# Kernel tuning notes

Measured on AMD Instinct MI355X. Metric: run time of the kernel, lower is better.

Reference implementation:

```python
import jax, jax.numpy as jnp
import numpy as np

MARGIN = 1.0
EPS = 1e-12


def setup_inputs() -> dict:
    key = jax.random.key(0)
    k1, k2 = jax.random.split(key)
    embeddings = jax.random.normal(k1, (4096, 768), dtype=jnp.float32)
    labels = jax.random.randint(k2, (4096,), 0, 4, dtype=jnp.int64)
    return {"embeddings": embeddings, "labels": labels}


def reference(embeddings, labels):
    # F.normalize(p=2, dim=1): x / max(||x||, eps)
    norm = jnp.linalg.norm(embeddings, axis=1, keepdims=True)
    e = embeddings / jnp.maximum(norm, EPS)

    # Euclidean pairwise distance matrix (not squared)
    dot = e @ e.T                                  # [N, N]
    sq = jnp.diagonal(dot)                         # [N]
    dist = sq[None, :] - 2.0 * dot + sq[:, None]
    dist = jnp.sqrt(jnp.maximum(dist, 0.0) + EPS)  # [N, N]

    # Masks: positives = same label, off-diagonal; negatives = different label
    n = labels.shape[0]
    eq = labels[None, :] == labels[:, None]
    pos_mask = eq & ~jnp.eye(n, dtype=bool)
    neg_mask = ~eq

    # Batch-hard mining: per-anchor hardest positive (masked max) and
    # hardest negative (masked min) -- replaces the per-row Python loop.
    d_ap = jnp.max(jnp.where(pos_mask, dist, -jnp.inf), axis=1)  # [N]
    d_an = jnp.min(jnp.where(neg_mask, dist, jnp.inf), axis=1)   # [N]

    valid = jnp.any(pos_mask, axis=1)  # anchors with at least one positive
    per_anchor = jnp.maximum(d_ap - d_an + MARGIN, 0.0)
    per_anchor = jnp.where(valid, per_anchor, 0.0)
    n_valid = jnp.maximum(jnp.sum(valid.astype(jnp.float32)), 1.0)
    return jnp.sum(per_anchor) / n_valid
```

## Files before the change

### kernel.cpp

```cpp
#include <hip/hip_runtime.h>
#include <math.h>

#define N 4096
#define D 768
#define MARGIN 1.0f
#define NTILE 1056
#define NKT 24
#define NSLOT 64

typedef _Float16 half8 __attribute__((ext_vector_type(8)));
typedef _Float16 half4 __attribute__((ext_vector_type(4)));
typedef float f32x4 __attribute__((ext_vector_type(4)));

__device__ __forceinline__ void gl2lds16(const void* g, void* l) {
    __builtin_amdgcn_global_load_lds((const __attribute__((address_space(1))) void*)g,
                                     (__attribute__((address_space(3))) void*)l, 16, 0, 0);
}

template<int Nv>
__device__ __forceinline__ void wait_vm() {
    if constexpr (Nv == 0)      asm volatile("s_waitcnt vmcnt(0)" ::: "memory");
    else if constexpr (Nv == 3) asm volatile("s_waitcnt vmcnt(3)" ::: "memory");
    else                        asm volatile("s_waitcnt vmcnt(6)" ::: "memory");
}

__global__ __launch_bounds__(256) void normalize_kernel(const float* __restrict__ x,
                                                        _Float16* __restrict__ e,
                                                        float* __restrict__ sq,
                                                        float* __restrict__ ap_part,
                                                        float* __restrict__ an_part,
                                                        float* __restrict__ acc,
                                                        unsigned* __restrict__ counter) {
    const int tid = threadIdx.x;
    const int wave = tid >> 6, lane = tid & 63;
    const int row = blockIdx.x * 4 + wave;

    const float4* xr = (const float4*)(x + (size_t)row * D);
    float4 f0 = xr[lane];
    float4 f1 = xr[lane + 64];
    float4 f2 = xr[lane + 128];

    float s = f0.x*f0.x + f0.y*f0.y + f0.z*f0.z + f0.w*f0.w
            + f1.x*f1.x + f1.y*f1.y + f1.z*f1.z + f1.w*f1.w
            + f2.x*f2.x + f2.y*f2.y + f2.z*f2.z + f2.w*f2.w;
    #pragma unroll
    for (int off = 1; off < 64; off <<= 1) s += __shfl_xor(s, off, 64);

    float scale = 1.0f / fmaxf(sqrtf(s), 1e-12f);

    half4* er = (half4*)(e + (size_t)row * D);
    half4 h0 = { (_Float16)(f0.x*scale), (_Float16)(f0.y*scale), (_Float16)(f0.z*scale), (_Float16)(f0.w*scale) };
    half4 h1 = { (_Float16)(f1.x*scale), (_Float16)(f1.y*scale), (_Float16)(f1.z*scale), (_Float16)(f1.w*scale) };
    half4 h2 = { (_Float16)(f2.x*scale), (_Float16)(f2.y*scale), (_Float16)(f2.z*scale), (_Float16)(f2.w*scale) };
    er[lane]       = h0;
    er[lane + 64]  = h1;
    er[lane + 128] = h2;

    if (lane == 0) sq[row] = s * scale * scale;

    int g = blockIdx.x * 256 + tid;
    ap_part[g] = 0.0f;
    an_part[g] = INFINITY;

    if (blockIdx.x == 0 && tid == 0) { acc[0] = 0.f; acc[1] = 0.f; *counter = 0u; }
}

__device__ __forceinline__ void stage_tile(const _Float16* __restrict__ e,
                                           int i0, int j0, int k0,
                                           unsigned short* Sb, int tid, int w) {
    #pragma unroll
    for (int p = 0; p < 2; ++p) {
        int s  = p * 256 + tid;
        int r  = s >> 2;
        int kg = (s & 3) ^ ((r >> 1) & 3);
        gl2lds16(e + (size_t)(i0 + r) * D + k0 + kg * 8,
                 (char*)Sb + (p * 256 + w * 64) * 16);
    }
    {
        int s  = tid;
        int r  = s >> 2;
        int kg = (s & 3) ^ ((r >> 1) & 3);
        gl2lds16(e + (size_t)(j0 + r) * D + k0 + kg * 8,
                 (char*)Sb + 8192 + (w * 64) * 16);
    }
}

__global__ __launch_bounds__(256, 4) void mine_kernel(const _Float16* __restrict__ e,
                                                      const float* __restrict__ sq,
                                                      const int* __restrict__ labels,
                                                      float* __restrict__ ap_part,
                                                      float* __restrict__ an_part) {
    __shared__ unsigned short S[3 * 6144];

    const int tid  = threadIdx.x;
    const int w    = tid >> 6;
    const int lane = tid & 63;
    const int ln15 = lane & 15;
    const int lq   = lane >> 4;
    const int wr   = w >> 1, wc = w & 1;
    const int wi   = wr * 64, wjL = wc * 32;

    const int b = (blockIdx.x & 7) * 132 + (blockIdx.x >> 3);

    int bi = 0, rem = b;
    while (rem >= 64 - 2 * bi) { rem -= 64 - 2 * bi; ++bi; }
    const int cj = 2 * bi + rem;
    const bool diag = (rem <= 1);
    const int i0 = bi * 128, j0 = cj * 64;

    f32x4 acc[4][2] = {};

    stage_tile(e, i0, j0, 0,  S,        tid, w);
    stage_tile(e, i0, j0, 32, S + 6144, tid, w);

    int cur = 0, nx2 = 2;
    for (int kt = 0; kt < NKT; ++kt) {
        if (kt < NKT - 1) wait_vm<3>(); else wait_vm<0>();
        __builtin_amdgcn_s_barrier();
        __builtin_amdgcn_sched_barrier(0);

        if (kt + 2 < NKT)
            stage_tile(e, i0, j0, (kt + 2) * 32, S + nx2 * 6144, tid, w);
        __builtin_amdgcn_sched_barrier(0);

        const unsigned short* Sb = S + cur * 6144;
        half8 af[4], bf[2];
        #pragma unroll
        for (int mt = 0; mt < 4; ++mt) {
            int r  = wi + mt * 16 + ln15;
            int kx = lq ^ ((r >> 1) & 3);
            af[mt] = *(const half8*)&Sb[r * 32 + kx * 8];
        }
        #pragma unroll
        for (int nt = 0; nt < 2; ++nt) {
            int c  = wjL + nt * 16 + ln15;
            int kx = lq ^ ((c >> 1) & 3);
            bf[nt] = *(const half8*)&Sb[4096 + c * 32 + kx * 8];
        }
        __builtin_amdgcn_s_setprio(1);
        #pragma unroll
        for (int mt = 0; mt < 4; ++mt)
            #pragma unroll
            for (int nt = 0; nt < 2; ++nt)
                acc[mt][nt] = __builtin_amdgcn_mfma_f32_16x16x32_f16(af[mt], bf[nt], acc[mt][nt], 0, 0, 0);
        __builtin_amdgcn_s_setprio(0);

        cur = (cur == 2) ? 0 : cur + 1;
        nx2 = (nx2 == 2) ? 0 : nx2 + 1;
    }

    float sqi[4][4]; int labi[4][4];
    #pragma unroll
    for (int mt = 0; mt < 4; ++mt)
        #pragma unroll
        for (int rg = 0; rg < 4; ++rg) {
            int i = i0 + wi + mt * 16 + lq * 4 + rg;
            sqi[mt][rg] = sq[i];
            labi[mt][rg] = labels[i];
        }
    float sqj[2]; int labj[2];
    #pragma unroll
    for (int nt = 0; nt < 2; ++nt) {
        int j = j0 + wjL + nt * 16 + ln15;
        sqj[nt] = sq[j];
        labj[nt] = labels[j];
    }

    float api[4][4], ani[4][4], apj[2], anj[2];
    #pragma unroll
    for (int mt = 0; mt < 4; ++mt)
        #pragma unroll
        for (int rg = 0; rg < 4; ++rg) { api[mt][rg] = -INFINITY; ani[mt][rg] = INFINITY; }
    #pragma unroll
    for (int nt = 0; nt < 2; ++nt) { apj[nt] = -INFINITY; anj[nt] = INFINITY; }

    #pragma unroll
    for (int nt = 0; nt < 2; ++nt) {
        int j = j0 + wjL + nt * 16 + ln15;
        #pragma unroll
        for (int mt = 0; mt < 4; ++mt)
            #pragma unroll
            for (int rg = 0; rg < 4; ++rg) {
                int i = i0 + wi + mt * 16 + lq * 4 + rg;
                float d2 = sqi[mt][rg] + sqj[nt] - 2.0f * acc[mt][nt][rg];
                float dist = sqrtf(fmaxf(d2, 0.0f) + 1e-12f);
                if (labi[mt][rg] == labj[nt]) {
                    if (i != j) {
                        api[mt][rg] = fmaxf(api[mt][rg], dist);
                        apj[nt]     = fmaxf(apj[nt], dist);
                    }
                } else {
                    ani[mt][rg] = fminf(ani[mt][rg], dist);
                    anj[nt]     = fminf(anj[nt], dist);
                }
            }
    }

    float* F = (float*)S;

    #pragma unroll
    for (int mt = 0; mt < 4; ++mt)
        #pragma unroll
        for (int rg = 0; rg < 4; ++rg) {
            float a_ = api[mt][rg], n_ = ani[mt][rg];
            #pragma unroll
            for (int off = 1; off < 16; off <<= 1) {
                a_ = fmaxf(a_, __shfl_xor(a_, off, 64));
                n_ = fminf(n_, __shfl_xor(n_, off, 64));
            }
            if (ln15 == 0) {
                int rl = mt * 16 + lq * 4 + rg;
                F[w * 128 + rl * 2]     = a_;
                F[w * 128 + rl * 2 + 1] = n_;
            }
        }
    __syncthreads();
    if (tid < 128) {
        int half = tid >> 6, rl = tid & 63;
        float a_ = fmaxf(F[(2 * half) * 128 + rl * 2],     F[(2 * half + 1) * 128 + rl * 2]);
        float n_ = fminf(F[(2 * half) * 128 + rl * 2 + 1], F[(2 * half + 1) * 128 + rl * 2 + 1]);
        int row = i0 + half * 64 + rl;
        ap_part[(size_t)cj * N + row] = a_;
        an_part[(size_t)cj * N + row] = n_;
    }

    if (!diag) {
        __syncthreads();
        #pragma unroll
        for (int nt = 0; nt < 2; ++nt) {
            float a_ = apj[nt], n_ = anj[nt];
            #pragma unroll
            for (int off = 16; off < 64; off <<= 1) {
                a_ = fmaxf(a_, __shfl_xor(a_, off, 64));
                n_ = fminf(n_, __shfl_xor(n_, off, 64));
            }
            if (lq == 0) {
                int jl = nt * 16 + ln15;
                F[w * 128 + jl * 2]     = a_;
                F[w * 128 + jl * 2 + 1] = n_;
            }
        }
        __syncthreads();
        if (tid < 64) {
            int wc2 = tid >> 5, jl = tid & 31;
            float a_ = fmaxf(F[wc2 * 128 + jl * 2],     F[(wc2 + 2) * 128 + jl * 2]);
            float n_ = fminf(F[wc2 * 128 + jl * 2 + 1], F[(wc2 + 2) * 128 + jl * 2 + 1]);
            int col = j0 + wc2 * 32 + jl;
            ap_part[(size_t)bi * N + col] = a_;
            an_part[(size_t)bi * N + col] = n_;
        }
    }
}

__global__ __launch_bounds__(256) void reduce_kernel(const float* __restrict__ ap_part,
                                                     const float* __restrict__ an_part,
                                                     const int* __restrict__ labels,
                                                     float* __restrict__ acc,
                                                     unsigned* __restrict__ counter,
                                                     float* __restrict__ out) {
    const int tid = threadIdx.x;
    const int rl  = tid & 63;
    const int q   = tid >> 6;
    const int r   = blockIdx.x * 64 + rl;

    __shared__ int cnt[4];
    __shared__ float Fa[4][64], Fn[4][64];
    if (tid < 4) cnt[tid] = 0;
    __syncthreads();
    int local[4] = {0, 0, 0, 0};
    for (int i = tid; i < N; i += 256) local[labels[i] & 3]++;
    #pragma unroll
    for (int c = 0; c < 4; c++) if (local[c]) atomicAdd(&cnt[c], local[c]);

    float ap = 0.0f, an = INFINITY;
    #pragma unroll
    for (int s = 0; s < 16; ++s) {
        int slot = q * 16 + s;
        ap = fmaxf(ap, ap_part[(size_t)slot * N + r]);
        an = fminf(an, an_part[(size_t)slot * N + r]);
    }
    Fa[q][rl] = ap; Fn[q][rl] = an;
    __syncthreads();

    if (tid < 64) {
        float a_ = fmaxf(fmaxf(Fa[0][tid], Fa[1][tid]), fmaxf(Fa[2][tid], Fa[3][tid]));
        float n_ = fminf(fminf(Fn[0][tid], Fn[1][tid]), fminf(Fn[2][tid], Fn[3][tid]));
        int row = blockIdx.x * 64 + tid;
        int l = labels[row] & 3;
        float sum = 0.f, nv = 0.f;
        if (cnt[l] >= 2) {
            nv = 1.f;
            if (n_ < 3.0e38f) sum = fmaxf(a_ - n_ + MARGIN, 0.f);
        }
        #pragma unroll
        for (int off = 32; off; off >>= 1) {
            sum += __shfl_down(sum, off, 64);
            nv  += __shfl_down(nv,  off, 64);
        }
        if (tid == 0) {
            atomicAdd(&acc[0], sum);
            atomicAdd(&acc[1], nv);
            __threadfence();
            if (atomicAdd(counter, 1u) == 63u) {
                float s_ = atomicAdd(&acc[0], 0.f);
                float nn = atomicAdd(&acc[1], 0.f);
                out[0] = s_ / fmaxf(nn, 1.f);
            }
        }
    }
}

extern "C" void kernel_launch(void* const* d_in, const int* in_sizes, int n_in,
                              void* d_out, int out_size, void* d_ws, size_t ws_size,
                              hipStream_t stream) {
    const float* x = (const float*)d_in[0];
    const int* labels = (const int*)d_in[1];
    float* out = (float*)d_out;

    _Float16* e = (_Float16*)d_ws;
    float* sq = (float*)(e + (size_t)N * D);
    float* ap_part = sq + N;
    float* an_part = ap_part + (size_t)NSLOT * N;
    float* acc = an_part + (size_t)NSLOT * N;
    unsigned* counter = (unsigned*)(acc + 2);

    normalize_kernel<<<N / 4, 256, 0, stream>>>(x, e, sq, ap_part, an_part, acc, counter);
    mine_kernel<<<NTILE, 256, 0, stream>>>(e, sq, labels, ap_part, an_part);
    reduce_kernel<<<N / 64, 256, 0, stream>>>(ap_part, an_part, labels, acc, counter, out);
}
```

Baseline: 116.5 us.

## Enlarge mining tiles to 128x128 with 8 waves and a 4-stage load pipeline

The mining kernel now covers the upper triangle with square 128x128 tiles computed by 512-thread blocks, instead of 128x64 tiles with 256 threads. This halves the tile count and the number of partial slots, and increases operand reuse per staged K-slice. The LDS ring grows from 3 to 4 buffers with a deeper prefetch distance, and the wait counts are adjusted to match. Because every partial slot is now written by either a row or a column write-back, the normalize kernel no longer initialises the partial buffers. In exchange, LDS use per block rises to 64KB and register pressure rises, which may limit how many blocks fit on each CU.

```diff
diff --git a/kernel.cpp b/kernel.cpp
--- a/kernel.cpp
+++ b/kernel.cpp
@@ -4,9 +4,9 @@
 #define N 4096
 #define D 768
 #define MARGIN 1.0f
-#define NTILE 1056
+#define NTILE 528
 #define NKT 24
-#define NSLOT 64
+#define NSLOT 32
 
 typedef _Float16 half8 __attribute__((ext_vector_type(8)));
 typedef _Float16 half4 __attribute__((ext_vector_type(4)));
@@ -20,15 +20,13 @@
 template<int Nv>
 __device__ __forceinline__ void wait_vm() {
     if constexpr (Nv == 0)      asm volatile("s_waitcnt vmcnt(0)" ::: "memory");
-    else if constexpr (Nv == 3) asm volatile("s_waitcnt vmcnt(3)" ::: "memory");
-    else                        asm volatile("s_waitcnt vmcnt(6)" ::: "memory");
+    else if constexpr (Nv == 2) asm volatile("s_waitcnt vmcnt(2)" ::: "memory");
+    else                        asm volatile("s_waitcnt vmcnt(4)" ::: "memory");
 }
 
 __global__ __launch_bounds__(256) void normalize_kernel(const float* __restrict__ x,
                                                         _Float16* __restrict__ e,
                                                         float* __restrict__ sq,
-                                                        float* __restrict__ ap_part,
-                                                        float* __restrict__ an_part,
                                                         float* __restrict__ acc,
                                                         unsigned* __restrict__ counter) {
     const int tid = threadIdx.x;
@@ -57,73 +55,68 @@
     er[lane + 128] = h2;
 
     if (lane == 0) sq[row] = s * scale * scale;
-
-    int g = blockIdx.x * 256 + tid;
-    ap_part[g] = 0.0f;
-    an_part[g] = INFINITY;
-
     if (blockIdx.x == 0 && tid == 0) { acc[0] = 0.f; acc[1] = 0.f; *counter = 0u; }
 }
 
 __device__ __forceinline__ void stage_tile(const _Float16* __restrict__ e,
                                            int i0, int j0, int k0,
-                                           unsigned short* Sb, int tid, int w) {
-    #pragma unroll
-    for (int p = 0; p < 2; ++p) {
-        int s  = p * 256 + tid;
-        int r  = s >> 2;
-        int kg = (s & 3) ^ ((r >> 1) & 3);
+                                           unsigned short* Sb, int tid) {
+    {
+        int r  = tid >> 2;
+        int kg = (tid & 3) ^ ((r >> 1) & 3);
         gl2lds16(e + (size_t)(i0 + r) * D + k0 + kg * 8,
-                 (char*)Sb + (p * 256 + w * 64) * 16);
+                 (char*)Sb + tid * 16);
     }
     {
-        int s  = tid;
-        int r  = s >> 2;
-        int kg = (s & 3) ^ ((r >> 1) & 3);
+        int r  = tid >> 2;
+        int kg = (tid & 3) ^ ((r >> 1) & 3);
         gl2lds16(e + (size_t)(j0 + r) * D + k0 + kg * 8,
-                 (char*)Sb + 8192 + (w * 64) * 16);
-    }
-}
-
-__global__ __launch_bounds__(256, 4) void mine_kernel(const _Float16* __restrict__ e,
+                 (char*)Sb + 8192 + tid * 16);
+    }
+}
+
+__global__ __launch_bounds__(512, 4) void mine_kernel(const _Float16* __restrict__ e,
                                                       const float* __restrict__ sq,
                                                       const int* __restrict__ labels,
                                                       float* __restrict__ ap_part,
                                                       float* __restrict__ an_part) {
-    __shared__ unsigned short S[3 * 6144];
+    __shared__ unsigned short S[4 * 8192];
 
     const int tid  = threadIdx.x;
     const int w    = tid >> 6;
     const int lane = tid & 63;
     const int ln15 = lane & 15;
     const int lq   = lane >> 4;
-    const int wr   = w >> 1, wc = w & 1;
+    const int wr   = w >> 2, wc = w & 3;
     const int wi   = wr * 64, wjL = wc * 32;
 
-    const int b = (blockIdx.x & 7) * 132 + (blockIdx.x >> 3);
+    const int b = (blockIdx.x & 7) * 66 + (blockIdx.x >> 3);
 
     int bi = 0, rem = b;
-    while (rem >= 64 - 2 * bi) { rem -= 64 - 2 * bi; ++bi; }
-    const int cj = 2 * bi + rem;
-    const bool diag = (rem <= 1);
-    const int i0 = bi * 128, j0 = cj * 64;
+    while (rem >= 32 - bi) { rem -= 32 - bi; ++bi; }
+    const int bj = bi + rem;
+    const bool diag = (bi == bj);
+    const int i0 = bi * 128, j0 = bj * 128;
 
     f32x4 acc[4][2] = {};
 
-    stage_tile(e, i0, j0, 0,  S,        tid, w);
-    stage_tile(e, i0, j0, 32, S + 6144, tid, w);
-
-    int cur = 0, nx2 = 2;
+    stage_tile(e, i0, j0, 0,  S,            tid);
+    stage_tile(e, i0, j0, 32, S + 8192,     tid);
+    stage_tile(e, i0, j0, 64, S + 2 * 8192, tid);
+
+    int cur = 0, nx3 = 3;
     for (int kt = 0; kt < NKT; ++kt) {
-        if (kt < NKT - 1) wait_vm<3>(); else wait_vm<0>();
+        if (kt < NKT - 2)      wait_vm<4>();
+        else if (kt == NKT - 2) wait_vm<2>();
+        else                    wait_vm<0>();
         __builtin_amdgcn_s_barrier();
         __builtin_amdgcn_sched_barrier(0);
 
-        if (kt + 2 < NKT)
-            stage_tile(e, i0, j0, (kt + 2) * 32, S + nx2 * 6144, tid, w);
+        if (kt + 3 < NKT)
+            stage_tile(e, i0, j0, (kt + 3) * 32, S + nx3 * 8192, tid);
         __builtin_amdgcn_sched_barrier(0);
 
-        const unsigned short* Sb = S + cur * 6144;
+        const unsigned short* Sb = S + cur * 8192;
         half8 af[4], bf[2];
         #pragma unroll
         for (int mt = 0; mt < 4; ++mt) {
@@ -145,8 +138,8 @@
                 acc[mt][nt] = __builtin_amdgcn_mfma_f32_16x16x32_f16(af[mt], bf[nt], acc[mt][nt], 0, 0, 0);
         __builtin_amdgcn_s_setprio(0);
 
-        cur = (cur == 2) ? 0 : cur + 1;
-        nx2 = (nx2 == 2) ? 0 : nx2 + 1;
+        cur = (cur + 1) & 3;
+        nx3 = (nx3 + 1) & 3;
     }
 
     float sqi[4][4]; int labi[4][4];
@@ -217,11 +210,14 @@
     __syncthreads();
     if (tid < 128) {
         int half = tid >> 6, rl = tid & 63;
-        float a_ = fmaxf(F[(2 * half) * 128 + rl * 2],     F[(2 * half + 1) * 128 + rl * 2]);
-        float n_ = fminf(F[(2 * half) * 128 + rl * 2 + 1], F[(2 * half + 1) * 128 + rl * 2 + 1]);
+        int wb = half * 4;
+        float a_ = fmaxf(fmaxf(F[(wb+0)*128 + rl*2], F[(wb+1)*128 + rl*2]),
+                         fmaxf(F[(wb+2)*128 + rl*2], F[(wb+3)*128 + rl*2]));
+        float n_ = fminf(fminf(F[(wb+0)*128 + rl*2+1], F[(wb+1)*128 + rl*2+1]),
+                         fminf(F[(wb+2)*128 + rl*2+1], F[(wb+3)*128 + rl*2+1]));
         int row = i0 + half * 64 + rl;
-        ap_part[(size_t)cj * N + row] = a_;
-        an_part[(size_t)cj * N + row] = n_;
+        ap_part[(size_t)bj * N + row] = a_;
+        an_part[(size_t)bj * N + row] = n_;
     }
 
     if (!diag) {
@@ -241,11 +237,11 @@
             }
         }
         __syncthreads();
-        if (tid < 64) {
+        if (tid < 128) {
             int wc2 = tid >> 5, jl = tid & 31;
-            float a_ = fmaxf(F[wc2 * 128 + jl * 2],     F[(wc2 + 2) * 128 + jl * 2]);
-            float n_ = fminf(F[wc2 * 128 + jl * 2 + 1], F[(wc2 + 2) * 128 + jl * 2 + 1]);
-            int col = j0 + wc2 * 32 + jl;
+            float a_ = fmaxf(F[wc2 * 128 + jl * 2],     F[(wc2 + 4) * 128 + jl * 2]);
+            float n_ = fminf(F[wc2 * 128 + jl * 2 + 1], F[(wc2 + 4) * 128 + jl * 2 + 1]);
+            int col = j0 + tid;
             ap_part[(size_t)bi * N + col] = a_;
             an_part[(size_t)bi * N + col] = n_;
         }
@@ -274,8 +270,8 @@
 
     float ap = 0.0f, an = INFINITY;
     #pragma unroll
-    for (int s = 0; s < 16; ++s) {
-        int slot = q * 16 + s;
+    for (int s = 0; s < 8; ++s) {
+        int slot = q * 8 + s;
         ap = fmaxf(ap, ap_part[(size_t)slot * N + r]);
         an = fminf(an, an_part[(size_t)slot * N + r]);
     }
@@ -324,7 +320,7 @@
     float* acc = an_part + (size_t)NSLOT * N;
     unsigned* counter = (unsigned*)(acc + 2);
 
-    normalize_kernel<<<N / 4, 256, 0, stream>>>(x, e, sq, ap_part, an_part, acc, counter);
-    mine_kernel<<<NTILE, 256, 0, stream>>>(e, sq, labels, ap_part, an_part);
+    normalize_kernel<<<N / 4, 256, 0, stream>>>(x, e, sq, acc, counter);
+    mine_kernel<<<NTILE, 512, 0, stream>>>(e, sq, labels, ap_part, an_part);
     reduce_kernel<<<N / 64, 256, 0, stream>>>(ap_part, an_part, labels, acc, counter, out);
 }
```

Measured after the change: 119.7 us. 1.03x slower.

## Load MFMA fragments directly from global into registers, dropping LDS staging

Applied to the files above, without the earlier changes.

Replaces the triple-buffered global-to-LDS staging with its barriers by direct per-wave global loads of half8 fragments into a two-stage register double buffer. The wave layout changes so each wave owns 32 rows by all 64 columns. This removes LDS traffic and per-k-step block barriers, and the row reduction now writes partials straight to global without a cross-wave LDS pass. The cost is redundant global/L2 reads: every wave reloads the full B tile and loads are no longer coalesced, so latency hiding depends on only two k-steps of prefetch.

```diff
diff --git a/kernel.cpp b/kernel.cpp
--- a/kernel.cpp
+++ b/kernel.cpp
@@ -12,17 +12,7 @@
 typedef _Float16 half4 __attribute__((ext_vector_type(4)));
 typedef float f32x4 __attribute__((ext_vector_type(4)));
 
-__device__ __forceinline__ void gl2lds16(const void* g, void* l) {
-    __builtin_amdgcn_global_load_lds((const __attribute__((address_space(1))) void*)g,
-                                     (__attribute__((address_space(3))) void*)l, 16, 0, 0);
-}
-
-template<int Nv>
-__device__ __forceinline__ void wait_vm() {
-    if constexpr (Nv == 0)      asm volatile("s_waitcnt vmcnt(0)" ::: "memory");
-    else if constexpr (Nv == 3) asm volatile("s_waitcnt vmcnt(3)" ::: "memory");
-    else                        asm volatile("s_waitcnt vmcnt(6)" ::: "memory");
-}
+#define LD8(p, off) (*(const half8*)((p) + (off)))
 
 __global__ __launch_bounds__(256) void normalize_kernel(const float* __restrict__ x,
                                                         _Float16* __restrict__ e,
@@ -65,40 +55,19 @@
     if (blockIdx.x == 0 && tid == 0) { acc[0] = 0.f; acc[1] = 0.f; *counter = 0u; }
 }
 
-__device__ __forceinline__ void stage_tile(const _Float16* __restrict__ e,
-                                           int i0, int j0, int k0,
-                                           unsigned short* Sb, int tid, int w) {
-    #pragma unroll
-    for (int p = 0; p < 2; ++p) {
-        int s  = p * 256 + tid;
-        int r  = s >> 2;
-        int kg = (s & 3) ^ ((r >> 1) & 3);
-        gl2lds16(e + (size_t)(i0 + r) * D + k0 + kg * 8,
-                 (char*)Sb + (p * 256 + w * 64) * 16);
-    }
-    {
-        int s  = tid;
-        int r  = s >> 2;
-        int kg = (s & 3) ^ ((r >> 1) & 3);
-        gl2lds16(e + (size_t)(j0 + r) * D + k0 + kg * 8,
-                 (char*)Sb + 8192 + (w * 64) * 16);
-    }
-}
-
 __global__ __launch_bounds__(256, 4) void mine_kernel(const _Float16* __restrict__ e,
                                                       const float* __restrict__ sq,
                                                       const int* __restrict__ labels,
                                                       float* __restrict__ ap_part,
                                                       float* __restrict__ an_part) {
-    __shared__ unsigned short S[3 * 6144];
+    __shared__ float F[4 * 128];
 
     const int tid  = threadIdx.x;
     const int w    = tid >> 6;
     const int lane = tid & 63;
     const int ln15 = lane & 15;
     const int lq   = lane >> 4;
-    const int wr   = w >> 1, wc = w & 1;
-    const int wi   = wr * 64, wjL = wc * 32;
+    const int wi   = w * 32;
 
     const int b = (blockIdx.x & 7) * 132 + (blockIdx.x >> 3);
 
@@ -108,77 +77,69 @@
     const bool diag = (rem <= 1);
     const int i0 = bi * 128, j0 = cj * 64;
 
-    f32x4 acc[4][2] = {};
-
-    stage_tile(e, i0, j0, 0,  S,        tid, w);
-    stage_tile(e, i0, j0, 32, S + 6144, tid, w);
-
-    int cur = 0, nx2 = 2;
+    const char* a0 = (const char*)(e + (size_t)(i0 + wi + ln15) * D) + lq * 16;
+    const char* a1 = a0 + 16 * (D * 2);
+    const char* b0 = (const char*)(e + (size_t)(j0 + ln15) * D) + lq * 16;
+    const char* b1 = b0 + 16 * (D * 2);
+    const char* b2 = b0 + 32 * (D * 2);
+    const char* b3 = b0 + 48 * (D * 2);
+
+    f32x4 acc[2][4] = {};
+    half8 fa[2][2], fb[2][4];
+
+    fa[0][0] = LD8(a0, 0);  fa[0][1] = LD8(a1, 0);
+    fb[0][0] = LD8(b0, 0);  fb[0][1] = LD8(b1, 0);
+    fb[0][2] = LD8(b2, 0);  fb[0][3] = LD8(b3, 0);
+    fa[1][0] = LD8(a0, 64); fa[1][1] = LD8(a1, 64);
+    fb[1][0] = LD8(b0, 64); fb[1][1] = LD8(b1, 64);
+    fb[1][2] = LD8(b2, 64); fb[1][3] = LD8(b3, 64);
+
+    #pragma unroll
     for (int kt = 0; kt < NKT; ++kt) {
-        if (kt < NKT - 1) wait_vm<3>(); else wait_vm<0>();
-        __builtin_amdgcn_s_barrier();
-        __builtin_amdgcn_sched_barrier(0);
-
-        if (kt + 2 < NKT)
-            stage_tile(e, i0, j0, (kt + 2) * 32, S + nx2 * 6144, tid, w);
-        __builtin_amdgcn_sched_barrier(0);
-
-        const unsigned short* Sb = S + cur * 6144;
-        half8 af[4], bf[2];
-        #pragma unroll
-        for (int mt = 0; mt < 4; ++mt) {
-            int r  = wi + mt * 16 + ln15;
-            int kx = lq ^ ((r >> 1) & 3);
-            af[mt] = *(const half8*)&Sb[r * 32 + kx * 8];
-        }
-        #pragma unroll
-        for (int nt = 0; nt < 2; ++nt) {
-            int c  = wjL + nt * 16 + ln15;
-            int kx = lq ^ ((c >> 1) & 3);
-            bf[nt] = *(const half8*)&Sb[4096 + c * 32 + kx * 8];
-        }
-        __builtin_amdgcn_s_setprio(1);
-        #pragma unroll
-        for (int mt = 0; mt < 4; ++mt)
-            #pragma unroll
-            for (int nt = 0; nt < 2; ++nt)
-                acc[mt][nt] = __builtin_amdgcn_mfma_f32_16x16x32_f16(af[mt], bf[nt], acc[mt][nt], 0, 0, 0);
-        __builtin_amdgcn_s_setprio(0);
-
-        cur = (cur == 2) ? 0 : cur + 1;
-        nx2 = (nx2 == 2) ? 0 : nx2 + 1;
-    }
-
-    float sqi[4][4]; int labi[4][4];
-    #pragma unroll
-    for (int mt = 0; mt < 4; ++mt)
+        const int cs = kt & 1;
+        #pragma unroll
+        for (int mt = 0; mt < 2; ++mt)
+            #pragma unroll
+            for (int nt = 0; nt < 4; ++nt)
+                acc[mt][nt] = __builtin_amdgcn_mfma_f32_16x16x32_f16(fa[cs][mt], fb[cs][nt], acc[mt][nt], 0, 0, 0);
+        if (kt + 2 < NKT) {
+            const int off = (kt + 2) * 64;
+            fa[cs][0] = LD8(a0, off); fa[cs][1] = LD8(a1, off);
+            fb[cs][0] = LD8(b0, off); fb[cs][1] = LD8(b1, off);
+            fb[cs][2] = LD8(b2, off); fb[cs][3] = LD8(b3, off);
+        }
+    }
+
+    float sqi[2][4]; int labi[2][4];
+    #pragma unroll
+    for (int mt = 0; mt < 2; ++mt)
         #pragma unroll
         for (int rg = 0; rg < 4; ++rg) {
             int i = i0 + wi + mt * 16 + lq * 4 + rg;
             sqi[mt][rg] = sq[i];
             labi[mt][rg] = labels[i];
         }
-    float sqj[2]; int labj[2];
-    #pragma unroll
-    for (int nt = 0; nt < 2; ++nt) {
-        int j = j0 + wjL + nt * 16 + ln15;
+    float sqj[4]; int labj[4];
+    #pragma unroll
+    for (int nt = 0; nt < 4; ++nt) {
+        int j = j0 + nt * 16 + ln15;
         sqj[nt] = sq[j];
         labj[nt] = labels[j];
     }
 
-    float api[4][4], ani[4][4], apj[2], anj[2];
-    #pragma unroll
-    for (int mt = 0; mt < 4; ++mt)
+    float api[2][4], ani[2][4], apj[4], anj[4];
+    #pragma unroll
+    for (int mt = 0; mt < 2; ++mt)
         #pragma unroll
         for (int rg = 0; rg < 4; ++rg) { api[mt][rg] = -INFINITY; ani[mt][rg] = INFINITY; }
     #pragma unroll
-    for (int nt = 0; nt < 2; ++nt) { apj[nt] = -INFINITY; anj[nt] = INFINITY; }
-
-    #pragma unroll
-    for (int nt = 0; nt < 2; ++nt) {
-        int j = j0 + wjL + nt * 16 + ln15;
-        #pragma unroll
-        for (int mt = 0; mt < 4; ++mt)
+    for (int nt = 0; nt < 4; ++nt) { apj[nt] = -INFINITY; anj[nt] = INFINITY; }
+
+    #pragma unroll
+    for (int nt = 0; nt < 4; ++nt) {
+        int j = j0 + nt * 16 + ln15;
+        #pragma unroll
+        for (int mt = 0; mt < 2; ++mt)
             #pragma unroll
             for (int rg = 0; rg < 4; ++rg) {
                 int i = i0 + wi + mt * 16 + lq * 4 + rg;
@@ -196,10 +157,8 @@
             }
     }
 
-    float* F = (float*)S;
-
-    #pragma unroll
-    for (int mt = 0; mt < 4; ++mt)
+    #pragma unroll
+    for (int mt = 0; mt < 2; ++mt)
         #pragma unroll
         for (int rg = 0; rg < 4; ++rg) {
             float a_ = api[mt][rg], n_ = ani[mt][rg];
@@ -209,25 +168,15 @@
                 n_ = fminf(n_, __shfl_xor(n_, off, 64));
             }
             if (ln15 == 0) {
-                int rl = mt * 16 + lq * 4 + rg;
-                F[w * 128 + rl * 2]     = a_;
-                F[w * 128 + rl * 2 + 1] = n_;
-            }
-        }
-    __syncthreads();
-    if (tid < 128) {
-        int half = tid >> 6, rl = tid & 63;
-        float a_ = fmaxf(F[(2 * half) * 128 + rl * 2],     F[(2 * half + 1) * 128 + rl * 2]);
-        float n_ = fminf(F[(2 * half) * 128 + rl * 2 + 1], F[(2 * half + 1) * 128 + rl * 2 + 1]);
-        int row = i0 + half * 64 + rl;
-        ap_part[(size_t)cj * N + row] = a_;
-        an_part[(size_t)cj * N + row] = n_;
-    }
+                int row = i0 + wi + mt * 16 + lq * 4 + rg;
+                ap_part[(size_t)cj * N + row] = a_;
+                an_part[(size_t)cj * N + row] = n_;
+            }
+        }
 
     if (!diag) {
-        __syncthreads();
-        #pragma unroll
-        for (int nt = 0; nt < 2; ++nt) {
+        #pragma unroll
+        for (int nt = 0; nt < 4; ++nt) {
             float a_ = apj[nt], n_ = anj[nt];
             #pragma unroll
             for (int off = 16; off < 64; off <<= 1) {
@@ -242,10 +191,11 @@
         }
         __syncthreads();
         if (tid < 64) {
-            int wc2 = tid >> 5, jl = tid & 31;
-            float a_ = fmaxf(F[wc2 * 128 + jl * 2],     F[(wc2 + 2) * 128 + jl * 2]);
-            float n_ = fminf(F[wc2 * 128 + jl * 2 + 1], F[(wc2 + 2) * 128 + jl * 2 + 1]);
-            int col = j0 + wc2 * 32 + jl;
+            float a_ = fmaxf(fmaxf(F[0 * 128 + tid * 2],     F[1 * 128 + tid * 2]),
+                             fmaxf(F[2 * 128 + tid * 2],     F[3 * 128 + tid * 2]));
+            float n_ = fminf(fminf(F[0 * 128 + tid * 2 + 1], F[1 * 128 + tid * 2 + 1]),
+                             fminf(F[2 * 128 + tid * 2 + 1], F[3 * 128 + tid * 2 + 1]));
+            int col = j0 + tid;
             ap_part[(size_t)bi * N + col] = a_;
             an_part[(size_t)bi * N + col] = n_;
         }
```

Result: slower. 166.6 us (+43.0%).
